# Kernel optimization log

Hardware: AMD Instinct MI355X
Metric: run time of the kernel (lower is better)

## Reference

```python
import jax, jax.numpy as jnp
import numpy as np
import math

S, B, D, H = 2048, 2, 1024, 16
HD = D // H  # head_dim = 64


def setup_inputs() -> dict:
    key = jax.random.key(0)
    ks = jax.random.split(key, 8)
    scale = 0.02
    return {
        "query": jax.random.normal(ks[0], (S, B, D), jnp.float32),
        "key": jax.random.normal(ks[1], (S, B, D), jnp.float32),
        "value": jax.random.normal(ks[2], (S, B, D), jnp.float32),
        "mask": jax.random.randint(ks[3], (1, S, 1, 1), 0, 2, jnp.int32),
        "w_q": jax.random.normal(ks[4], (D, D), jnp.float32) * scale,
        "b_q": jnp.zeros((D,), jnp.float32),
        "w_k": jax.random.normal(ks[5], (D, D), jnp.float32) * scale,
        "b_k": jnp.zeros((D,), jnp.float32),
        "w_v": jax.random.normal(ks[6], (D, D), jnp.float32) * scale,
        "b_v": jnp.zeros((D,), jnp.float32),
    }


def reference(query, key, value, mask, w_q, b_q, w_k, b_k, w_v, b_v):
    # Linear projections (torch Linear: x @ W^T + b); inputs are (S, B, D)
    q = query @ w_q.T + b_q
    k = key @ w_k.T + b_k
    v = value @ w_v.T + b_v
    # split heads: (S, B, H, HD)
    q = q.reshape(S, B, H, HD)
    k = k.reshape(S, B, H, HD)
    v = v.reshape(S, B, H, HD)
    # scores over (query_i, key_j, batch, head)
    scores = jnp.einsum("ibhd,jbhd->ijbh", q, k) * (1.0 / math.sqrt(HD))
    # mask (1, S, 1, 1) broadcasts against (i, j, b, h); 0 => masked
    scores = jnp.where(mask == 0, -jnp.inf, scores)
    # softmax over key axis j (original: nn.Softmax(dim=1))
    attn = jax.nn.softmax(scores, axis=1)
    out = jnp.einsum("ijbh,jbhd->ibhd", attn, v)  # (S, B, H, HD)
    return out.reshape(S, B, D)
```

## Files before the change

### kernel.cpp

```cpp
#include <hip/hip_runtime.h>
#include <stdint.h>


#define S_ 2048
#define B_ 2
#define D_ 1024
#define H_ 16
#define HD_ 64
#define M_ (S_ * B_)

typedef __bf16 bf16;
typedef bf16 bf16x8 __attribute__((ext_vector_type(8)));
typedef float floatx4 __attribute__((ext_vector_type(4)));

#define QSCALE 0.18033688011112042f

__device__ __forceinline__ void async_cp16(const bf16* g, bf16* l) {
    __builtin_amdgcn_global_load_lds(
        (const __attribute__((address_space(1))) void*)g,
        (__attribute__((address_space(3))) void*)l, 16, 0, 0);
}

__global__ __launch_bounds__(256) void mask_scan(const int* __restrict__ mask,
                                                 int* __restrict__ sidx,
                                                 int* __restrict__ cnt)
{
    __shared__ int sums[256];
    const int tid = threadIdx.x;
    int v[8], s = 0;
    #pragma unroll
    for (int j = 0; j < 8; j++) { v[j] = mask[tid * 8 + j] ? 1 : 0; s += v[j]; }
    sums[tid] = s;
    __syncthreads();
    for (int off = 1; off < 256; off <<= 1) {
        int t = (tid >= off) ? sums[tid - off] : 0;
        __syncthreads();
        sums[tid] += t;
        __syncthreads();
    }
    int base = (tid > 0) ? sums[tid - 1] : 0;
    #pragma unroll
    for (int j = 0; j < 8; j++)
        if (v[j]) { sidx[base] = tid * 8 + j; base++; }
    if (tid == 255) cnt[0] = sums[255];
}

__global__ __launch_bounds__(256) void cvt_gather(
    const float* __restrict__ xq, const float* __restrict__ xk, const float* __restrict__ xv,
    const int* __restrict__ sidx, const int* __restrict__ cnt,
    bf16* __restrict__ oq, bf16* __restrict__ ok, bf16* __restrict__ ov)
{
    const int z = blockIdx.y;
    const float* src = (z == 0) ? xq : (z == 1) ? xk : xv;
    bf16*        dst = (z == 0) ? oq : (z == 1) ? ok : ov;

    const int tid = threadIdx.x;
    const int rm  = blockIdx.x * 2 + (tid >> 7);
    int srow = rm;
    if (z != 0) {
        const int cs = rm >> 1, b = rm & 1;
        if (cs >= cnt[0]) return;
        srow = sidx[cs] * 2 + b;
    }
    const int col = (tid & 127) * 8;
    const floatx4* sp = (const floatx4*)(src + (size_t)srow * D_ + col);
    floatx4 x0 = sp[0], x1 = sp[1];
    bf16x8 v;
    #pragma unroll
    for (int j = 0; j < 4; j++) { v[j] = (bf16)x0[j]; v[4 + j] = (bf16)x1[j]; }
    *(bf16x8*)(dst + (size_t)rm * D_ + col) = v;
}

__global__ __launch_bounds__(256) void cvt3(
    const float* __restrict__ a, const float* __restrict__ b, const float* __restrict__ c,
    bf16* __restrict__ oa, bf16* __restrict__ ob, bf16* __restrict__ oc)
{
    const int z = blockIdx.z;
    const float* src = (z == 0) ? a : (z == 1) ? b : c;
    bf16*        dst = (z == 0) ? oa : (z == 1) ? ob : oc;
    const size_t i = ((size_t)blockIdx.x * 256 + threadIdx.x) * 8;
    floatx4 x0 = *(const floatx4*)(src + i);
    floatx4 x1 = *(const floatx4*)(src + i + 4);
    bf16x8 v;
    #pragma unroll
    for (int j = 0; j < 4; j++) { v[j] = (bf16)x0[j]; v[4 + j] = (bf16)x1[j]; }
    *(bf16x8*)(dst + i) = v;
}

#define TM 128
#define TN 128
#define BK 32

__global__ __launch_bounds__(256) void qkv_gemm_async(
    const bf16* __restrict__ xq, const bf16* __restrict__ xk, const bf16* __restrict__ xv,
    const bf16* __restrict__ wq, const bf16* __restrict__ wk, const bf16* __restrict__ wv,
    const float* __restrict__ bq, const float* __restrict__ bk, const float* __restrict__ bv,
    const int* __restrict__ cnt,
    bf16* __restrict__ oq, bf16* __restrict__ ok, bf16* __restrict__ ov)
{
    __shared__ __align__(16) bf16 a_lds[TM * BK];
    __shared__ __align__(16) bf16 b_lds[TN * BK];

    const int z = blockIdx.y;
    const bf16*  X  = (z == 0) ? xq : (z == 1) ? xk : xv;
    const bf16*  W  = (z == 0) ? wq : (z == 1) ? wk : wv;
    const float* Bi = (z == 0) ? bq : (z == 1) ? bk : bv;
    bf16*        O  = (z == 0) ? oq : (z == 1) ? ok : ov;

    const int f   = blockIdx.x;
    const int xcd = f & 7, t = f >> 3;
    const int m0  = ((t & 3) * 8 + xcd) * TM;
    const int n0  = (t >> 2) * TN;

    const int rows_active = (z == 0) ? M_ : 2 * cnt[0];
    if (m0 >= rows_active) return;

    const int tid  = threadIdx.x;
    const int wid  = tid >> 6;
    const int lane = tid & 63;
    const int wm = wid >> 1, wn = wid & 1;
    const int lm = lane & 15, lq = lane >> 4;

    const bf16* src_a = (z == 2) ? b_lds : a_lds;
    const bf16* src_b = (z == 2) ? a_lds : b_lds;
    const int a_base = ((z == 2) ? wn : wm) * 64;
    const int b_base = ((z == 2) ? wm : wn) * 64;

    floatx4 acc[4][4] = {};

    for (int kt = 0; kt < D_; kt += BK) {
        __syncthreads();
        #pragma unroll
        for (int tt = 0; tt < 2; tt++) {
            const int cb = (tt * 4 + wid) * 64;
            const int c  = cb + lane;
            const int row = c >> 2, kc = c & 3;
            async_cp16(X + (size_t)(m0 + row) * D_ + kt + kc * 8, a_lds + cb * 8);
            async_cp16(W + (size_t)(n0 + row) * D_ + kt + kc * 8, b_lds + cb * 8);
        }
        __syncthreads();

        bf16x8 af[4], bfv[4];
        #pragma unroll
        for (int i = 0; i < 4; i++)
            af[i] = *(const bf16x8*)(src_a + (a_base + i * 16 + lm) * BK + lq * 8);
        #pragma unroll
        for (int j = 0; j < 4; j++)
            bfv[j] = *(const bf16x8*)(src_b + (b_base + j * 16 + lm) * BK + lq * 8);
        #pragma unroll
        for (int i = 0; i < 4; i++)
            #pragma unroll
            for (int j = 0; j < 4; j++)
                acc[i][j] = __builtin_amdgcn_mfma_f32_16x16x32_bf16(
                    af[i], bfv[j], acc[i][j], 0, 0, 0);
    }

    if (z != 2) {
        #pragma unroll
        for (int j = 0; j < 4; j++) {
            const int n = n0 + wn * 64 + j * 16 + lm;
            const float bias = Bi[n];
            const int h = n >> 6, hd = n & 63;
            #pragma unroll
            for (int i = 0; i < 4; i++) {
                const int mb = m0 + wm * 64 + i * 16 + lq * 4;
                #pragma unroll
                for (int r = 0; r < 4; r++) {
                    const int m = mb + r;
                    const int row = m >> 1, b = m & 1;
                    float v = acc[i][j][r] + bias;
                    if (z == 0) v *= QSCALE;
                    O[(((size_t)(b * H_ + h)) * S_ + row) * HD_ + hd] = (bf16)v;
                }
            }
        }
    } else {
        #pragma unroll
        for (int j = 0; j < 4; j++) {
            const int m = m0 + wm * 64 + j * 16 + lm;
            const int cs = m >> 1, b = m & 1;
            #pragma unroll
            for (int i = 0; i < 4; i++) {
                const int wb = n0 + wn * 64 + i * 16 + lq * 4;
                #pragma unroll
                for (int r = 0; r < 4; r++) {
                    const int n = wb + r;
                    const float bias = Bi[n];
                    const int h = n >> 6, d = n & 63;
                    O[(((size_t)(b * H_ + h)) * HD_ + d) * S_ + cs] =
                        (bf16)(acc[i][j][r] + bias);
                }
            }
        }
    }
}

#define KT 64

__global__ __launch_bounds__(256) void attn_kernel(
    const bf16* __restrict__ qw, const bf16* __restrict__ kw, const bf16* __restrict__ vtw,
    const int* __restrict__ cnt, float* __restrict__ out)
{
    __shared__ __align__(16) bf16 k_lds[KT * HD_];
    __shared__ __align__(16) bf16 v_ldsT[HD_ * KT];
    __shared__ __align__(16) bf16 p_lds[4 * 16 * 72];

    const int tid  = threadIdx.x;
    const int wid  = tid >> 6;
    const int lane = tid & 63;
    const int lm = lane & 15, lq = lane >> 4;
    const int bh = blockIdx.y;
    const int q0 = blockIdx.x * 64;
    const int count = cnt[0];

    const bf16* Qb  = qw  + (size_t)bh * S_ * HD_;
    const bf16* Kb  = kw  + (size_t)bh * S_ * HD_;
    const bf16* VTb = vtw + (size_t)bh * HD_ * S_;

    bf16x8 qf[2];
    {
        const bf16* qp = Qb + (size_t)(q0 + wid * 16 + lm) * HD_;
        qf[0] = *(const bf16x8*)(qp + lq * 8);
        qf[1] = *(const bf16x8*)(qp + 32 + lq * 8);
    }

    float lsum[4] = {0.f, 0.f, 0.f, 0.f};
    floatx4 oacc[4] = {};
    bf16* pw = p_lds + wid * 16 * 72;

    for (int j0 = 0; j0 < count; j0 += KT) {
        __syncthreads();

        #pragma unroll
        for (int c = tid; c < KT * 8; c += 256) {
            const int row = c >> 3, ch = c & 7;
            bf16x8 kv = *(const bf16x8*)(Kb + (size_t)(j0 + row) * HD_ + ch * 8);
            *(bf16x8*)(k_lds + row * 64 + ((ch ^ (row & 7)) * 8)) = kv;
        }
        #pragma unroll
        for (int c = tid; c < KT * 8; c += 256) {
            const int d = c >> 3, ch = c & 7;
            bf16x8 vv = *(const bf16x8*)(VTb + (size_t)d * S_ + j0 + ch * 8);
            *(bf16x8*)(v_ldsT + d * 64 + ((ch ^ (d & 7)) * 8)) = vv;
        }
        __syncthreads();

        floatx4 sacc[4] = {};
        #pragma unroll
        for (int ks = 0; ks < 2; ks++)
            #pragma unroll
            for (int n = 0; n < 4; n++) {
                bf16x8 kf = *(const bf16x8*)(k_lds + (n * 16 + lm) * 64 +
                                             (((ks * 4 + lq) ^ (lm & 7)) * 8));
                sacc[n] = __builtin_amdgcn_mfma_f32_16x16x32_bf16(qf[ks], kf, sacc[n], 0, 0, 0);
            }

        float valf[4];
        #pragma unroll
        for (int n = 0; n < 4; n++)
            valf[n] = (j0 + n * 16 + lm < count) ? 1.0f : 0.0f;

        #pragma unroll
        for (int r = 0; r < 4; r++)
            #pragma unroll
            for (int n = 0; n < 4; n++) {
                const float p = exp2f(sacc[n][r]) * valf[n];
                lsum[r] += p;
                pw[(lq * 4 + r) * 72 + n * 16 + lm] = (bf16)p;
            }
        __syncthreads();

        #pragma unroll
        for (int ks = 0; ks < 2; ks++) {
            bf16x8 pf = *(const bf16x8*)(pw + lm * 72 + ks * 32 + lq * 8);
            #pragma unroll
            for (int n = 0; n < 4; n++) {
                bf16x8 vf = *(const bf16x8*)(v_ldsT + (n * 16 + lm) * 64 +
                                             (((ks * 4 + lq) ^ (lm & 7)) * 8));
                oacc[n] = __builtin_amdgcn_mfma_f32_16x16x32_bf16(pf, vf, oacc[n], 0, 0, 0);
            }
        }
    }

    float invl[4];
    #pragma unroll
    for (int r = 0; r < 4; r++) {
        float lr = lsum[r];
        lr += __shfl_xor(lr, 1);
        lr += __shfl_xor(lr, 2);
        lr += __shfl_xor(lr, 4);
        lr += __shfl_xor(lr, 8);
        invl[r] = 1.0f / lr;
    }
    const int b = bh >> 4, h = bh & 15;
    #pragma unroll
    for (int n = 0; n < 4; n++)
        #pragma unroll
        for (int r = 0; r < 4; r++) {
            const int q = q0 + wid * 16 + lq * 4 + r;
            out[((size_t)q * B_ + b) * D_ + h * 64 + n * 16 + lm] = oacc[n][r] * invl[r];
        }
}

extern "C" void kernel_launch(void* const* d_in, const int* in_sizes, int n_in,
                              void* d_out, int out_size, void* d_ws, size_t ws_size,
                              hipStream_t stream) {
    const float* xq = (const float*)d_in[0];
    const float* xk = (const float*)d_in[1];
    const float* xv = (const float*)d_in[2];
    const int*  mask = (const int*)d_in[3];
    const float* wq = (const float*)d_in[4];
    const float* bq = (const float*)d_in[5];
    const float* wk = (const float*)d_in[6];
    const float* bk = (const float*)d_in[7];
    const float* wv = (const float*)d_in[8];
    const float* bv = (const float*)d_in[9];

    const size_t NX = (size_t)M_ * D_;
    const size_t NW = (size_t)D_ * D_;
    char* ws = (char*)d_ws;
    int* cnt  = (int*)ws;
    int* sidx = cnt + 16;
    char* base = ws + 16384;

    bf16* xqb = (bf16*)base;
    bf16* xkb = xqb + NX;
    bf16* xvb = xkb + NX;
    bf16* wqb = xvb + NX;
    bf16* wkb = wqb + NW;
    bf16* wvb = wkb + NW;
    bf16* q_ws  = wvb + NW;
    bf16* k_ws  = q_ws + NX;
    bf16* vt_ws = k_ws + NX;

    mask_scan<<<1, 256, 0, stream>>>(mask, sidx, cnt);
    cvt_gather<<<dim3(M_ / 2, 3), 256, 0, stream>>>(xq, xk, xv, sidx, cnt,
                                                    xqb, xkb, xvb);
    cvt3<<<dim3(NW / 2048, 1, 3), 256, 0, stream>>>(wq, wk, wv, wqb, wkb, wvb);

    qkv_gemm_async<<<dim3(256, 3), 256, 0, stream>>>(xqb, xkb, xvb, wqb, wkb, wvb,
                                                     bq, bk, bv, cnt,
                                                     q_ws, k_ws, vt_ws);

    attn_kernel<<<dim3(S_ / 64, B_ * H_), 256, 0, stream>>>(q_ws, k_ws, vt_ws,
                                                            cnt, (float*)d_out);
}
```

Measured before the change: 209.2 us.

## Pre-tile compacted K/V in MFMA fragment layout and load attention operands directly

The mask scan now produces per-row compacted positions instead of an index list. The input conversion runs as a single plain kernel with no gather. The QKV GEMM uses 128x64 tiles with an LDS swizzle and XCD-aware block mapping. Its epilogue scatters unmasked K and V rows directly into 64-key tiles arranged in MFMA fragment order. The attention kernel then loads K and V fragments straight from global memory, with no LDS staging or barriers, and also uses an XCD-aware grid. The trade-off is that K and V projections are computed for all rows, including masked ones, so GEMM work is no longer reduced by the mask.

```diff
diff --git a/kernel.cpp b/kernel.cpp
--- a/kernel.cpp
+++ b/kernel.cpp
@@ -21,8 +21,10 @@
         (__attribute__((address_space(3))) void*)l, 16, 0, 0);
 }
 
+#define TILE_OFF(bh, tile) (((size_t)(bh) * 32 + (tile)) * 4096)
+
 __global__ __launch_bounds__(256) void mask_scan(const int* __restrict__ mask,
-                                                 int* __restrict__ sidx,
+                                                 int* __restrict__ pos,
                                                  int* __restrict__ cnt)
 {
     __shared__ int sums[256];
@@ -40,93 +42,65 @@
     }
     int base = (tid > 0) ? sums[tid - 1] : 0;
     #pragma unroll
-    for (int j = 0; j < 8; j++)
-        if (v[j]) { sidx[base] = tid * 8 + j; base++; }
+    for (int j = 0; j < 8; j++) { pos[tid * 8 + j] = base; base += v[j]; }
     if (tid == 255) cnt[0] = sums[255];
 }
 
-__global__ __launch_bounds__(256) void cvt_gather(
-    const float* __restrict__ xq, const float* __restrict__ xk, const float* __restrict__ xv,
-    const int* __restrict__ sidx, const int* __restrict__ cnt,
-    bf16* __restrict__ oq, bf16* __restrict__ ok, bf16* __restrict__ ov)
+__global__ __launch_bounds__(256) void cvt6(
+    const float* __restrict__ x0, const float* __restrict__ x1, const float* __restrict__ x2,
+    const float* __restrict__ w0, const float* __restrict__ w1, const float* __restrict__ w2,
+    bf16* __restrict__ o0, bf16* __restrict__ o1, bf16* __restrict__ o2,
+    bf16* __restrict__ o3, bf16* __restrict__ o4, bf16* __restrict__ o5)
 {
     const int z = blockIdx.y;
-    const float* src = (z == 0) ? xq : (z == 1) ? xk : xv;
-    bf16*        dst = (z == 0) ? oq : (z == 1) ? ok : ov;
-
-    const int tid = threadIdx.x;
-    const int rm  = blockIdx.x * 2 + (tid >> 7);
-    int srow = rm;
-    if (z != 0) {
-        const int cs = rm >> 1, b = rm & 1;
-        if (cs >= cnt[0]) return;
-        srow = sidx[cs] * 2 + b;
-    }
-    const int col = (tid & 127) * 8;
-    const floatx4* sp = (const floatx4*)(src + (size_t)srow * D_ + col);
-    floatx4 x0 = sp[0], x1 = sp[1];
+    if (z >= 3 && blockIdx.x >= 512) return;
+    const float* src = (z == 0) ? x0 : (z == 1) ? x1 : (z == 2) ? x2
+                     : (z == 3) ? w0 : (z == 4) ? w1 : w2;
+    bf16* dst = (z == 0) ? o0 : (z == 1) ? o1 : (z == 2) ? o2
+              : (z == 3) ? o3 : (z == 4) ? o4 : o5;
+    const size_t i = ((size_t)blockIdx.x * 256 + threadIdx.x) * 8;
+    floatx4 a = *(const floatx4*)(src + i);
+    floatx4 b = *(const floatx4*)(src + i + 4);
     bf16x8 v;
     #pragma unroll
-    for (int j = 0; j < 4; j++) { v[j] = (bf16)x0[j]; v[4 + j] = (bf16)x1[j]; }
-    *(bf16x8*)(dst + (size_t)rm * D_ + col) = v;
-}
-
-__global__ __launch_bounds__(256) void cvt3(
-    const float* __restrict__ a, const float* __restrict__ b, const float* __restrict__ c,
-    bf16* __restrict__ oa, bf16* __restrict__ ob, bf16* __restrict__ oc)
-{
-    const int z = blockIdx.z;
-    const float* src = (z == 0) ? a : (z == 1) ? b : c;
-    bf16*        dst = (z == 0) ? oa : (z == 1) ? ob : oc;
-    const size_t i = ((size_t)blockIdx.x * 256 + threadIdx.x) * 8;
-    floatx4 x0 = *(const floatx4*)(src + i);
-    floatx4 x1 = *(const floatx4*)(src + i + 4);
-    bf16x8 v;
-    #pragma unroll
-    for (int j = 0; j < 4; j++) { v[j] = (bf16)x0[j]; v[4 + j] = (bf16)x1[j]; }
+    for (int j = 0; j < 4; j++) { v[j] = (bf16)a[j]; v[4 + j] = (bf16)b[j]; }
     *(bf16x8*)(dst + i) = v;
 }
 
 #define TM 128
-#define TN 128
+#define TN 64
 #define BK 32
 
-__global__ __launch_bounds__(256) void qkv_gemm_async(
+__global__ __launch_bounds__(256, 4) void qkv_gemm_async(
     const bf16* __restrict__ xq, const bf16* __restrict__ xk, const bf16* __restrict__ xv,
     const bf16* __restrict__ wq, const bf16* __restrict__ wk, const bf16* __restrict__ wv,
     const float* __restrict__ bq, const float* __restrict__ bk, const float* __restrict__ bv,
-    const int* __restrict__ cnt,
+    const int* __restrict__ mask, const int* __restrict__ pos,
     bf16* __restrict__ oq, bf16* __restrict__ ok, bf16* __restrict__ ov)
 {
     __shared__ __align__(16) bf16 a_lds[TM * BK];
     __shared__ __align__(16) bf16 b_lds[TN * BK];
 
-    const int z = blockIdx.y;
+    const int fid = blockIdx.x;
+    const int xcd = fid & 7;
+    const int t   = fid >> 3;
+    const int z   = t >> 6;
+    const int u   = t & 63;
+    const int m0  = ((u & 3) * 8 + xcd) * TM;
+    const int n0  = (u >> 2) * TN;
+
     const bf16*  X  = (z == 0) ? xq : (z == 1) ? xk : xv;
     const bf16*  W  = (z == 0) ? wq : (z == 1) ? wk : wv;
     const float* Bi = (z == 0) ? bq : (z == 1) ? bk : bv;
-    bf16*        O  = (z == 0) ? oq : (z == 1) ? ok : ov;
-
-    const int f   = blockIdx.x;
-    const int xcd = f & 7, t = f >> 3;
-    const int m0  = ((t & 3) * 8 + xcd) * TM;
-    const int n0  = (t >> 2) * TN;
-
-    const int rows_active = (z == 0) ? M_ : 2 * cnt[0];
-    if (m0 >= rows_active) return;
 
     const int tid  = threadIdx.x;
     const int wid  = tid >> 6;
     const int lane = tid & 63;
     const int wm = wid >> 1, wn = wid & 1;
     const int lm = lane & 15, lq = lane >> 4;
-
-    const bf16* src_a = (z == 2) ? b_lds : a_lds;
-    const bf16* src_b = (z == 2) ? a_lds : b_lds;
-    const int a_base = ((z == 2) ? wn : wm) * 64;
-    const int b_base = ((z == 2) ? wm : wn) * 64;
-
-    floatx4 acc[4][4] = {};
+    const int ksw = lq ^ ((lm >> 1) & 3);
+
+    floatx4 acc[4][2] = {};
 
     for (int kt = 0; kt < D_; kt += BK) {
         __syncthreads();
@@ -134,92 +108,85 @@
         for (int tt = 0; tt < 2; tt++) {
             const int cb = (tt * 4 + wid) * 64;
             const int c  = cb + lane;
-            const int row = c >> 2, kc = c & 3;
+            const int row = c >> 2, kc = (c & 3) ^ ((c >> 3) & 3);
             async_cp16(X + (size_t)(m0 + row) * D_ + kt + kc * 8, a_lds + cb * 8);
+        }
+        {
+            const int cb = wid * 64;
+            const int c  = cb + lane;
+            const int row = c >> 2, kc = (c & 3) ^ ((c >> 3) & 3);
             async_cp16(W + (size_t)(n0 + row) * D_ + kt + kc * 8, b_lds + cb * 8);
         }
         __syncthreads();
 
-        bf16x8 af[4], bfv[4];
+        bf16x8 af[4], bf[2];
         #pragma unroll
         for (int i = 0; i < 4; i++)
-            af[i] = *(const bf16x8*)(src_a + (a_base + i * 16 + lm) * BK + lq * 8);
-        #pragma unroll
-        for (int j = 0; j < 4; j++)
-            bfv[j] = *(const bf16x8*)(src_b + (b_base + j * 16 + lm) * BK + lq * 8);
+            af[i] = *(const bf16x8*)(a_lds + (wm * 64 + i * 16 + lm) * 32 + ksw * 8);
+        #pragma unroll
+        for (int j = 0; j < 2; j++)
+            bf[j] = *(const bf16x8*)(b_lds + (wn * 32 + j * 16 + lm) * 32 + ksw * 8);
         #pragma unroll
         for (int i = 0; i < 4; i++)
             #pragma unroll
-            for (int j = 0; j < 4; j++)
+            for (int j = 0; j < 2; j++)
                 acc[i][j] = __builtin_amdgcn_mfma_f32_16x16x32_bf16(
-                    af[i], bfv[j], acc[i][j], 0, 0, 0);
-    }
-
-    if (z != 2) {
-        #pragma unroll
-        for (int j = 0; j < 4; j++) {
-            const int n = n0 + wn * 64 + j * 16 + lm;
-            const float bias = Bi[n];
-            const int h = n >> 6, hd = n & 63;
-            #pragma unroll
-            for (int i = 0; i < 4; i++) {
-                const int mb = m0 + wm * 64 + i * 16 + lq * 4;
-                #pragma unroll
-                for (int r = 0; r < 4; r++) {
-                    const int m = mb + r;
-                    const int row = m >> 1, b = m & 1;
-                    float v = acc[i][j][r] + bias;
-                    if (z == 0) v *= QSCALE;
-                    O[(((size_t)(b * H_ + h)) * S_ + row) * HD_ + hd] = (bf16)v;
+                    af[i], bf[j], acc[i][j], 0, 0, 0);
+    }
+
+    #pragma unroll
+    for (int j = 0; j < 2; j++) {
+        const int n = n0 + wn * 32 + j * 16 + lm;
+        const float bias = Bi[n];
+        const int h = n >> 6, hd = n & 63;
+        #pragma unroll
+        for (int i = 0; i < 4; i++) {
+            const int mb = m0 + wm * 64 + i * 16 + lq * 4;
+            #pragma unroll
+            for (int r = 0; r < 4; r++) {
+                const int m = mb + r;
+                const int s = m >> 1, b = m & 1;
+                const float v = acc[i][j][r] + bias;
+                const int bh = b * H_ + h;
+                if (z == 0) {
+                    oq[((size_t)bh * S_ + s) * HD_ + hd] = (bf16)(v * QSCALE);
+                } else if (mask[s]) {
+                    const int cs = pos[s];
+                    if (z == 1) {
+                        ok[TILE_OFF(bh, cs >> 6) + (hd >> 3) * 512 +
+                           (cs & 63) * 8 + (hd & 7)] = (bf16)v;
+                    } else {
+                        ov[TILE_OFF(bh, cs >> 6) + ((cs >> 3) & 7) * 512 +
+                           hd * 8 + (cs & 7)] = (bf16)v;
+                    }
                 }
             }
         }
-    } else {
-        #pragma unroll
-        for (int j = 0; j < 4; j++) {
-            const int m = m0 + wm * 64 + j * 16 + lm;
-            const int cs = m >> 1, b = m & 1;
-            #pragma unroll
-            for (int i = 0; i < 4; i++) {
-                const int wb = n0 + wn * 64 + i * 16 + lq * 4;
-                #pragma unroll
-                for (int r = 0; r < 4; r++) {
-                    const int n = wb + r;
-                    const float bias = Bi[n];
-                    const int h = n >> 6, d = n & 63;
-                    O[(((size_t)(b * H_ + h)) * HD_ + d) * S_ + cs] =
-                        (bf16)(acc[i][j][r] + bias);
-                }
-            }
-        }
-    }
-}
-
-#define KT 64
-
-__global__ __launch_bounds__(256) void attn_kernel(
+    }
+}
+
+__global__ __launch_bounds__(256, 4) void attn_kernel(
     const bf16* __restrict__ qw, const bf16* __restrict__ kw, const bf16* __restrict__ vtw,
     const int* __restrict__ cnt, float* __restrict__ out)
 {
-    __shared__ __align__(16) bf16 k_lds[KT * HD_];
-    __shared__ __align__(16) bf16 v_ldsT[HD_ * KT];
     __shared__ __align__(16) bf16 p_lds[4 * 16 * 72];
+
+    const int fid  = blockIdx.x;
+    const int xcd  = fid & 7;
+    const int t    = fid >> 3;
+    const int bh   = (t & 3) * 8 + xcd;
+    const int q0   = (t >> 2) * 64;
 
     const int tid  = threadIdx.x;
     const int wid  = tid >> 6;
     const int lane = tid & 63;
     const int lm = lane & 15, lq = lane >> 4;
-    const int bh = blockIdx.y;
-    const int q0 = blockIdx.x * 64;
     const int count = cnt[0];
-
-    const bf16* Qb  = qw  + (size_t)bh * S_ * HD_;
-    const bf16* Kb  = kw  + (size_t)bh * S_ * HD_;
-    const bf16* VTb = vtw + (size_t)bh * HD_ * S_;
+    const int ntiles = (count + 63) >> 6;
 
     bf16x8 qf[2];
     {
-        const bf16* qp = Qb + (size_t)(q0 + wid * 16 + lm) * HD_;
+        const bf16* qp = qw + ((size_t)bh * S_ + q0 + wid * 16 + lm) * HD_;
         qf[0] = *(const bf16x8*)(qp + lq * 8);
         qf[1] = *(const bf16x8*)(qp + 32 + lq * 8);
     }
@@ -228,57 +195,59 @@
     floatx4 oacc[4] = {};
     bf16* pw = p_lds + wid * 16 * 72;
 
-    for (int j0 = 0; j0 < count; j0 += KT) {
-        __syncthreads();
-
-        #pragma unroll
-        for (int c = tid; c < KT * 8; c += 256) {
-            const int row = c >> 3, ch = c & 7;
-            bf16x8 kv = *(const bf16x8*)(Kb + (size_t)(j0 + row) * HD_ + ch * 8);
-            *(bf16x8*)(k_lds + row * 64 + ((ch ^ (row & 7)) * 8)) = kv;
-        }
-        #pragma unroll
-        for (int c = tid; c < KT * 8; c += 256) {
-            const int d = c >> 3, ch = c & 7;
-            bf16x8 vv = *(const bf16x8*)(VTb + (size_t)d * S_ + j0 + ch * 8);
-            *(bf16x8*)(v_ldsT + d * 64 + ((ch ^ (d & 7)) * 8)) = vv;
-        }
-        __syncthreads();
+    for (int tl = 0; tl < ntiles; tl++) {
+        const size_t tbase = TILE_OFF(bh, tl);
+        const size_t foff  = (size_t)lq * 512 + (size_t)lm * 8;
+
+        bf16x8 kf[2][4];
+        #pragma unroll
+        for (int ks = 0; ks < 2; ks++)
+            #pragma unroll
+            for (int n = 0; n < 4; n++)
+                kf[ks][n] = *(const bf16x8*)(kw + tbase + ks * 2048 + foff + n * 128);
 
         floatx4 sacc[4] = {};
         #pragma unroll
         for (int ks = 0; ks < 2; ks++)
             #pragma unroll
-            for (int n = 0; n < 4; n++) {
-                bf16x8 kf = *(const bf16x8*)(k_lds + (n * 16 + lm) * 64 +
-                                             (((ks * 4 + lq) ^ (lm & 7)) * 8));
-                sacc[n] = __builtin_amdgcn_mfma_f32_16x16x32_bf16(qf[ks], kf, sacc[n], 0, 0, 0);
-            }
-
+            for (int n = 0; n < 4; n++)
+                sacc[n] = __builtin_amdgcn_mfma_f32_16x16x32_bf16(
+                    qf[ks], kf[ks][n], sacc[n], 0, 0, 0);
+
+        const int jb = tl * 64;
         float valf[4];
         #pragma unroll
         for (int n = 0; n < 4; n++)
-            valf[n] = (j0 + n * 16 + lm < count) ? 1.0f : 0.0f;
-
+            valf[n] = (jb + n * 16 + lm < count) ? 1.0f : 0.0f;
         #pragma unroll
         for (int r = 0; r < 4; r++)
             #pragma unroll
             for (int n = 0; n < 4; n++) {
                 const float p = exp2f(sacc[n][r]) * valf[n];
                 lsum[r] += p;
-                pw[(lq * 4 + r) * 72 + n * 16 + lm] = (bf16)p;
+                sacc[n][r] = p;
             }
-        __syncthreads();
+
+        bf16x8 vf[2][4];
+        #pragma unroll
+        for (int ks = 0; ks < 2; ks++)
+            #pragma unroll
+            for (int n = 0; n < 4; n++)
+                vf[ks][n] = *(const bf16x8*)(vtw + tbase + ks * 2048 + foff + n * 128);
+
+        #pragma unroll
+        for (int r = 0; r < 4; r++)
+            #pragma unroll
+            for (int n = 0; n < 4; n++)
+                pw[(lq * 4 + r) * 72 + n * 16 + lm] = (bf16)sacc[n][r];
 
         #pragma unroll
         for (int ks = 0; ks < 2; ks++) {
             bf16x8 pf = *(const bf16x8*)(pw + lm * 72 + ks * 32 + lq * 8);
             #pragma unroll
-            for (int n = 0; n < 4; n++) {
-                bf16x8 vf = *(const bf16x8*)(v_ldsT + (n * 16 + lm) * 64 +
-                                             (((ks * 4 + lq) ^ (lm & 7)) * 8));
-                oacc[n] = __builtin_amdgcn_mfma_f32_16x16x32_bf16(pf, vf, oacc[n], 0, 0, 0);
-            }
+            for (int n = 0; n < 4; n++)
+                oacc[n] = __builtin_amdgcn_mfma_f32_16x16x32_bf16(
+                    pf, vf[ks][n], oacc[n], 0, 0, 0);
         }
     }
 
@@ -319,8 +288,8 @@
     const size_t NX = (size_t)M_ * D_;
     const size_t NW = (size_t)D_ * D_;
     char* ws = (char*)d_ws;
-    int* cnt  = (int*)ws;
-    int* sidx = cnt + 16;
+    int* cnt = (int*)ws;
+    int* pos = cnt + 16;
     char* base = ws + 16384;
 
     bf16* xqb = (bf16*)base;
@@ -333,15 +302,11 @@
     bf16* k_ws  = q_ws + NX;
     bf16* vt_ws = k_ws + NX;
 
-    mask_scan<<<1, 256, 0, stream>>>(mask, sidx, cnt);
-    cvt_gather<<<dim3(M_ / 2, 3), 256, 0, stream>>>(xq, xk, xv, sidx, cnt,
-                                                    xqb, xkb, xvb);
-    cvt3<<<dim3(NW / 2048, 1, 3), 256, 0, stream>>>(wq, wk, wv, wqb, wkb, wvb);
-
-    qkv_gemm_async<<<dim3(256, 3), 256, 0, stream>>>(xqb, xkb, xvb, wqb, wkb, wvb,
-                                                     bq, bk, bv, cnt,
-                                                     q_ws, k_ws, vt_ws);
-
-    attn_kernel<<<dim3(S_ / 64, B_ * H_), 256, 0, stream>>>(q_ws, k_ws, vt_ws,
-                                                            cnt, (float*)d_out);
-}
+    mask_scan<<<1, 256, 0, stream>>>(mask, pos, cnt);
+    cvt6<<<dim3(2048, 6), 256, 0, stream>>>(xq, xk, xv, wq, wk, wv,
+                                            xqb, xkb, xvb, wqb, wkb, wvb);
+    qkv_gemm_async<<<1536, 256, 0, stream>>>(xqb, xkb, xvb, wqb, wkb, wvb,
+                                             bq, bk, bv, mask, pos,
+                                             q_ws, k_ws, vt_ws);
+    attn_kernel<<<1024, 256, 0, stream>>>(q_ws, k_ws, vt_ws, cnt, (float*)d_out);
+}
```

Result: no change. 211.2 us (+1.0%).
